# Kernel optimization log

Hardware: AMD Instinct MI355X
Metric: run time of the kernel (lower is better)

The kernel has to match this reference:

```python
import jax, jax.numpy as jnp
import numpy as np

D_MODEL = 512
N_HEADS = 8
B, T = 2, 2048
EPS = 1e-6


def _phi(x):
    # ELU feature map: elu(x) + 1 (always positive)
    return jax.nn.elu(x) + 1.0


def setup_inputs() -> dict:
    key = jax.random.key(0)
    ks = jax.random.split(key, 9)
    s = 1.0 / np.sqrt(D_MODEL)
    x = jax.random.normal(ks[0], (B, T, D_MODEL), dtype=jnp.float32)
    Wq = jax.random.uniform(ks[1], (D_MODEL, D_MODEL), jnp.float32, -s, s)
    bq = jax.random.uniform(ks[2], (D_MODEL,), jnp.float32, -s, s)
    Wk = jax.random.uniform(ks[3], (D_MODEL, D_MODEL), jnp.float32, -s, s)
    bk = jax.random.uniform(ks[4], (D_MODEL,), jnp.float32, -s, s)
    Wv = jax.random.uniform(ks[5], (D_MODEL, D_MODEL), jnp.float32, -s, s)
    bv = jax.random.uniform(ks[6], (D_MODEL,), jnp.float32, -s, s)
    Wo = jax.random.uniform(ks[7], (D_MODEL, D_MODEL), jnp.float32, -s, s)
    bo = jax.random.uniform(ks[8], (D_MODEL,), jnp.float32, -s, s)
    return {"x": x, "Wq": Wq, "bq": bq, "Wk": Wk, "bk": bk,
            "Wv": Wv, "bv": bv, "Wo": Wo, "bo": bo}


def reference(x, Wq, bq, Wk, bk, Wv, bv, Wo, bo):
    Bb, Tt, _ = x.shape
    H = N_HEADS
    D = D_MODEL // H

    def heads(W, b):
        # (B,T,d_model) -> (B,H,T,D)
        return (x @ W + b).reshape(Bb, Tt, H, D).transpose(0, 2, 1, 3)

    Q = _phi(heads(Wq, bq))
    K = _phi(heads(Wk, bk))
    V = heads(Wv, bv)

    # Causal linear attention: S_t = sum_{j<=t} phi(K_j) ⊗ V_j, z_t = sum_{j<=t} phi(K_j)
    KV = jnp.einsum('bhtd,bhtm->bhtdm', K, V)   # (B,H,T,D,D)
    S = jnp.cumsum(KV, axis=2)
    z = jnp.cumsum(K, axis=2)
    num = jnp.einsum('bhtd,bhtdm->bhtm', Q, S)  # (B,H,T,D)
    den = jnp.maximum(jnp.einsum('bhtd,bhtd->bht', Q, z), EPS)[..., None]
    out = num / den

    out = out.transpose(0, 2, 1, 3).reshape(Bb, Tt, D_MODEL)
    return out @ Wo + bo
```

## Files before the change

### kernel.cpp

```cpp
#include <hip/hip_runtime.h>
#include <math.h>

#define DM 512
#define NH 8
#define HD 64
#define BB 2
#define TT 2048
#define CHUNK 64
#define NC (TT / CHUNK)
#define BH (BB * NH)
#define ROWS (BB * TT)
#define EPSV 1e-6f

typedef short bf16x8 __attribute__((ext_vector_type(8)));
typedef float f32x4 __attribute__((ext_vector_type(4)));
typedef unsigned short us;

union U4 { us h[4]; uint2 u; };

__device__ __forceinline__ us f2bf(float f) {
    unsigned int u = __float_as_uint(f);
    return (us)((u + 0x7FFFu + ((u >> 16) & 1u)) >> 16);
}
__device__ __forceinline__ float bf2f(us h) {
    return __uint_as_float(((unsigned int)h) << 16);
}
__device__ __forceinline__ void gload16(const void* g, void* l) {
    __builtin_amdgcn_global_load_lds(
        (const __attribute__((address_space(1))) unsigned int*)g,
        (__attribute__((address_space(3))) unsigned int*)l, 16, 0, 0);
}
#define SWZ(r, k) ((k) ^ (((r) & 7) << 3))

__global__ __launch_bounds__(256) void prep(
    const float* __restrict__ x,
    const float* __restrict__ Wq, const float* __restrict__ Wk,
    const float* __restrict__ Wv, const float* __restrict__ Wo,
    us* __restrict__ xb, us* __restrict__ WT)
{
    const int bid = blockIdx.x, tid = threadIdx.x;
    __shared__ float tl[32][33];
    if (bid < 2048) {
        const int i = bid * 256 + tid;
        float4 v = ((const float4*)x)[i];
        U4 o;
        o.h[0] = f2bf(v.x); o.h[1] = f2bf(v.y);
        o.h[2] = f2bf(v.z); o.h[3] = f2bf(v.w);
        ((uint2*)xb)[i] = o.u;
    } else {
        const int b2 = bid - 2048;
        const int which = b2 >> 8, t = b2 & 255;
        const float* W = (which == 0) ? Wq : (which == 1) ? Wk : (which == 2) ? Wv : Wo;
        us* O = WT + (size_t)which * DM * DM;
        const int r0 = (t >> 4) * 32, c0 = (t & 15) * 32;
        const int tr = tid >> 3, tc = tid & 7;
        float4 v = *(const float4*)&W[(size_t)(r0 + tr) * DM + c0 + tc * 4];
        tl[tr][tc * 4 + 0] = v.x; tl[tr][tc * 4 + 1] = v.y;
        tl[tr][tc * 4 + 2] = v.z; tl[tr][tc * 4 + 3] = v.w;
        __syncthreads();
        U4 o;
#pragma unroll
        for (int i = 0; i < 4; ++i) o.h[i] = f2bf(tl[tc * 4 + i][tr]);
        *(uint2*)&O[(size_t)(c0 + tr) * DM + r0 + tc * 4] = o.u;
    }
}

__device__ __forceinline__ void stage_tiles(
    const us* __restrict__ Ag, const us* __restrict__ Bg,
    int r0, int c0, int k0, int tid, us* As, us* Bs)
{
    const int fa = tid * 8;
#pragma unroll
    for (int i = 0; i < 2; ++i) {
        const int f = fa + i * 2048, row = f >> 6, kp = f & 63;
        gload16(Ag + (size_t)(r0 + row) * DM + k0 + SWZ(row, kp), As + f);
    }
#pragma unroll
    for (int i = 0; i < 4; ++i) {
        const int f = fa + i * 2048, row = f >> 6, kp = f & 63;
        gload16(Bg + (size_t)(c0 + row) * DM + k0 + SWZ(row, kp), Bs + f);
    }
}

__device__ __forceinline__ void gemm64x128(
    const us* __restrict__ Ag, const us* __restrict__ Bg,
    int r0, int c0, int tid, us* Asl, us* Bsl, f32x4 (&acc)[2][4])
{
    const int lane = tid & 63, wid = tid >> 6;
    const int wr = wid >> 1, wc = wid & 1;
    const int lrow = lane & 15, lk8 = (lane >> 4) * 8;

    stage_tiles(Ag, Bg, r0, c0, 0, tid, Asl, Bsl);
    __syncthreads();
    int cur = 0;
    for (int k0 = 0; k0 < DM; k0 += 64) {
        if (k0 + 64 < DM)
            stage_tiles(Ag, Bg, r0, c0, k0 + 64, tid,
                        Asl + (cur ^ 1) * 4096, Bsl + (cur ^ 1) * 8192);
        const us* As = Asl + cur * 4096;
        const us* Bs = Bsl + cur * 8192;
#pragma unroll
        for (int kin = 0; kin < 64; kin += 32) {
            bf16x8 af[2], bfr[4];
#pragma unroll
            for (int mi = 0; mi < 2; ++mi) {
                const int row = wr * 32 + mi * 16 + lrow;
                af[mi] = *(const bf16x8*)&As[row * 64 + SWZ(row, kin + lk8)];
            }
#pragma unroll
            for (int ni = 0; ni < 4; ++ni) {
                const int row = wc * 64 + ni * 16 + lrow;
                bfr[ni] = *(const bf16x8*)&Bs[row * 64 + SWZ(row, kin + lk8)];
            }
#pragma unroll
            for (int mi = 0; mi < 2; ++mi)
#pragma unroll
                for (int ni = 0; ni < 4; ++ni)
                    acc[mi][ni] = __builtin_amdgcn_mfma_f32_16x16x32_bf16(
                        af[mi], bfr[ni], acc[mi][ni], 0, 0, 0);
        }
        __syncthreads();
        cur ^= 1;
    }
}

__global__ __launch_bounds__(256) void qkv_mfma(
    const us* __restrict__ xb, const us* __restrict__ WT,
    const float* __restrict__ bq, const float* __restrict__ bk,
    const float* __restrict__ bv,
    us* __restrict__ qn, us* __restrict__ kn,
    us* __restrict__ kt, us* __restrict__ vt)
{
    const int which = blockIdx.z;
    const us* Bg = WT + (size_t)which * DM * DM;
    const float* bias = (which == 0) ? bq : (which == 1) ? bk : bv;

    __shared__ us Asl[2 * 4096];
    __shared__ us Bsl[2 * 8192];
    f32x4 acc[2][4] = {};
    const int r0 = blockIdx.x * 64, c0 = blockIdx.y * 128;
    const int tid = threadIdx.x;

    gemm64x128(xb, Bg, r0, c0, tid, Asl, Bsl, acc);

    const int lane = tid & 63, wid = tid >> 6;
    const int wr = wid >> 1, wc = wid & 1;
    const int lrow = lane & 15, lr4 = (lane >> 4) * 4;
    const int b = r0 >> 11;

#pragma unroll
    for (int mi = 0; mi < 2; ++mi) {
        const int rowb = r0 + wr * 32 + mi * 16 + lr4;
        const int t0g = rowb & (TT - 1);
#pragma unroll
        for (int ni = 0; ni < 4; ++ni) {
            const int col = c0 + wc * 64 + ni * 16 + lrow;
            const int h = col >> 6, d = col & 63;
            const float bc = bias[col];
            U4 p4;
#pragma unroll
            for (int r = 0; r < 4; ++r) {
                float y = acc[mi][ni][r] + bc;
                if (which < 2) y = (y > 0.f) ? (y + 1.f) : __expf(y);
                const us hb = f2bf(y);
                p4.h[r] = hb;
                if (which == 0)
                    qn[((size_t)(b * NH + h) * TT + t0g + r) * HD + d] = hb;
                else if (which == 1)
                    kn[((size_t)(b * NH + h) * TT + t0g + r) * HD + d] = hb;
            }
            if (which == 1)
                *(uint2*)&kt[((size_t)(b * NH + h) * HD + d) * TT + t0g] = p4.u;
            else if (which == 2)
                *(uint2*)&vt[((size_t)(b * NH + h) * HD + d) * TT + t0g] = p4.u;
        }
    }
}

__global__ __launch_bounds__(256) void out_mfma(
    const us* __restrict__ Ag, const us* __restrict__ WoT,
    const float* __restrict__ bias, float* __restrict__ out)
{
    __shared__ us Asl[2 * 4096];
    __shared__ us Bsl[2 * 8192];
    f32x4 acc[2][4] = {};
    const int r0 = blockIdx.x * 64, c0 = blockIdx.y * 128;
    const int tid = threadIdx.x;

    gemm64x128(Ag, WoT, r0, c0, tid, Asl, Bsl, acc);

    const int lane = tid & 63, wid = tid >> 6;
    const int wr = wid >> 1, wc = wid & 1;
    const int lrow = lane & 15, lr4 = (lane >> 4) * 4;

#pragma unroll
    for (int mi = 0; mi < 2; ++mi)
#pragma unroll
        for (int ni = 0; ni < 4; ++ni) {
            const int col = c0 + wc * 64 + ni * 16 + lrow;
            const float bc = bias[col];
#pragma unroll
            for (int r = 0; r < 4; ++r) {
                const int row = r0 + wr * 32 + mi * 16 + lr4 + r;
                out[(size_t)row * DM + col] = acc[mi][ni][r] + bc;
            }
        }
}

__global__ __launch_bounds__(256) void chunk_sums(
    const us* __restrict__ kt, const us* __restrict__ vt,
    us* __restrict__ kvc, float* __restrict__ zc)
{
    const int blk = blockIdx.x, bh = blk >> 5, c = blk & 31;
    const int t0 = c * CHUNK;
    __shared__ us Ksl[4096], Vsl[4096];
    __shared__ float partial[4][64];
    const int tid = threadIdx.x;
    const us* ktb = kt + (size_t)bh * HD * TT;
    const us* vtb = vt + (size_t)bh * HD * TT;

#pragma unroll
    for (int i = 0; i < 2; ++i) {
        const int f = tid * 8 + i * 2048, row = f >> 6, kp = f & 63;
        const int kl = SWZ(row, kp);
        gload16(ktb + (size_t)row * TT + t0 + kl, Ksl + f);
        gload16(vtb + (size_t)row * TT + t0 + kl, Vsl + f);
    }
    __syncthreads();

    const int lane = tid & 63, wid = tid >> 6;
    const int wr = wid >> 1, wc = wid & 1;
    const int lrow = lane & 15, lk8 = (lane >> 4) * 8, lr4 = (lane >> 4) * 4;

    f32x4 acc[2][2] = {};
#pragma unroll
    for (int kin = 0; kin < 64; kin += 32) {
        bf16x8 af[2], bfr[2];
#pragma unroll
        for (int mi = 0; mi < 2; ++mi) {
            const int row = wr * 32 + mi * 16 + lrow;
            af[mi] = *(const bf16x8*)&Vsl[row * 64 + SWZ(row, kin + lk8)];
        }
#pragma unroll
        for (int ni = 0; ni < 2; ++ni) {
            const int row = wc * 32 + ni * 16 + lrow;
            bfr[ni] = *(const bf16x8*)&Ksl[row * 64 + SWZ(row, kin + lk8)];
        }
#pragma unroll
        for (int mi = 0; mi < 2; ++mi)
#pragma unroll
            for (int ni = 0; ni < 2; ++ni)
                acc[mi][ni] = __builtin_amdgcn_mfma_f32_16x16x32_bf16(
                    af[mi], bfr[ni], acc[mi][ni], 0, 0, 0);
    }

    us* dst = kvc + (size_t)blk * 4096;
#pragma unroll
    for (int mi = 0; mi < 2; ++mi)
#pragma unroll
        for (int ni = 0; ni < 2; ++ni) {
            const int d2 = wr * 32 + mi * 16 + lr4;
            const int d1 = wc * 32 + ni * 16 + lrow;
#pragma unroll
            for (int r = 0; r < 4; ++r)
                dst[(d2 + r) * 64 + d1] = f2bf(acc[mi][ni][r]);
        }

    {
        const int p = tid >> 6, d = tid & 63;
        float s = 0.f;
#pragma unroll
        for (int j = 0; j < 16; ++j)
            s += bf2f(Ksl[d * 64 + SWZ(d, p * 16 + j)]);
        partial[p][d] = s;
    }
    __syncthreads();
    if (tid < 64)
        zc[(size_t)blk * 64 + tid] =
            partial[0][tid] + partial[1][tid] + partial[2][tid] + partial[3][tid];
}

__global__ __launch_bounds__(256) void scan(
    const us* __restrict__ kvc, const float* __restrict__ zc,
    us* __restrict__ spr, float* __restrict__ zpr)
{
    const int bh = blockIdx.x, seg = blockIdx.y, tid = threadIdx.x;
    if (seg < 8) {
        const int e = seg * 512 + tid * 2;
        const size_t base = (size_t)(bh * NC) * 4096 + e;
        unsigned u[NC];
#pragma unroll
        for (int c = 0; c < NC; ++c)
            u[c] = *(const unsigned*)(kvc + base + (size_t)c * 4096);
        float r0 = 0.f, r1 = 0.f;
#pragma unroll
        for (int c = 0; c < NC; ++c) {
            const unsigned p = (unsigned)f2bf(r0) | ((unsigned)f2bf(r1) << 16);
            *(unsigned*)(spr + base + (size_t)c * 4096) = p;
            r0 += bf2f((us)(u[c] & 0xFFFF));
            r1 += bf2f((us)(u[c] >> 16));
        }
    } else if (tid < 64) {
        const size_t base = (size_t)(bh * NC) * 64 + tid;
        float zv[NC];
#pragma unroll
        for (int c = 0; c < NC; ++c) zv[c] = zc[base + (size_t)c * 64];
        float run = 0.f;
#pragma unroll
        for (int c = 0; c < NC; ++c) {
            zpr[base + (size_t)c * 64] = run;
            run += zv[c];
        }
    }
}

__global__ __launch_bounds__(256) void chunk_attn(
    const us* __restrict__ qn, const us* __restrict__ kn,
    const us* __restrict__ vt, const us* __restrict__ spr,
    const float* __restrict__ zpr, us* __restrict__ attn)
{
    const int blk = blockIdx.x, bh = blk >> 5, c = blk & 31;
    const int t0 = c * CHUNK;
    __shared__ us Qs[4096], Kns[4096], Vts[4096], Sts[4096], Abf[4096];
    __shared__ float zp[64], den[64], part[4][64];
    const int tid = threadIdx.x;

    const us* qb = qn + ((size_t)bh * TT + t0) * HD;
    const us* kb = kn + ((size_t)bh * TT + t0) * HD;
    const us* vb = vt + (size_t)bh * HD * TT;
    const us* sb = spr + (size_t)blk * 4096;

#pragma unroll
    for (int i = 0; i < 2; ++i) {
        const int f = tid * 8 + i * 2048, row = f >> 6, kp = f & 63;
        const int kl = SWZ(row, kp);
        gload16(qb + (size_t)row * HD + kl, Qs + f);
        gload16(kb + (size_t)row * HD + kl, Kns + f);
        gload16(vb + (size_t)row * TT + t0 + kl, Vts + f);
        gload16(sb + (size_t)row * 64 + kl, Sts + f);
    }
    if (tid < 64) zp[tid] = zpr[(size_t)blk * 64 + tid];
    __syncthreads();

    const int lane = tid & 63, wid = tid >> 6;
    const int wr = wid >> 1, wc = wid & 1;
    const int lrow = lane & 15, lk8 = (lane >> 4) * 8, lr4 = (lane >> 4) * 4;

    f32x4 accs[2][2] = {};
#pragma unroll
    for (int kin = 0; kin < 64; kin += 32) {
        bf16x8 af[2], bfr[2];
#pragma unroll
        for (int mi = 0; mi < 2; ++mi) {
            const int row = wr * 32 + mi * 16 + lrow;
            af[mi] = *(const bf16x8*)&Qs[row * 64 + SWZ(row, kin + lk8)];
        }
#pragma unroll
        for (int ni = 0; ni < 2; ++ni) {
            const int row = wc * 32 + ni * 16 + lrow;
            bfr[ni] = *(const bf16x8*)&Kns[row * 64 + SWZ(row, kin + lk8)];
        }
#pragma unroll
        for (int mi = 0; mi < 2; ++mi)
#pragma unroll
            for (int ni = 0; ni < 2; ++ni)
                accs[mi][ni] = __builtin_amdgcn_mfma_f32_16x16x32_bf16(
                    af[mi], bfr[ni], accs[mi][ni], 0, 0, 0);
    }

#pragma unroll
    for (int mi = 0; mi < 2; ++mi)
#pragma unroll
        for (int ni = 0; ni < 2; ++ni) {
            const int j = wc * 32 + ni * 16 + lrow;
#pragma unroll
            for (int r = 0; r < 4; ++r) {
                const int i = wr * 32 + mi * 16 + lr4 + r;
                const float v = (j <= i) ? accs[mi][ni][r] : 0.f;
                Abf[i * 64 + SWZ(i, j)] = f2bf(v);
            }
        }
    __syncthreads();

    {
        const int p = tid >> 6, i = tid & 63;
        float s = 0.f;
#pragma unroll
        for (int jj = 0; jj < 16; ++jj) {
            const int j = p * 16 + jj;
            s += bf2f(Abf[i * 64 + SWZ(i, j)]);
            s += bf2f(Qs[i * 64 + SWZ(i, j)]) * zp[j];
        }
        part[p][i] = s;
    }
    __syncthreads();
    if (tid < 64)
        den[tid] = fmaxf(part[0][tid] + part[1][tid] + part[2][tid] + part[3][tid], EPSV);
    __syncthreads();

    f32x4 acco[2][2] = {};
#pragma unroll
    for (int kin = 0; kin < 64; kin += 32) {
        bf16x8 af[2], bfr[2], ag[2], bgr[2];
#pragma unroll
        for (int mi = 0; mi < 2; ++mi) {
            const int row = wr * 32 + mi * 16 + lrow;
            af[mi] = *(const bf16x8*)&Abf[row * 64 + SWZ(row, kin + lk8)];
            ag[mi] = *(const bf16x8*)&Qs[row * 64 + SWZ(row, kin + lk8)];
        }
#pragma unroll
        for (int ni = 0; ni < 2; ++ni) {
            const int row = wc * 32 + ni * 16 + lrow;
            bfr[ni] = *(const bf16x8*)&Vts[row * 64 + SWZ(row, kin + lk8)];
            bgr[ni] = *(const bf16x8*)&Sts[row * 64 + SWZ(row, kin + lk8)];
        }
#pragma unroll
        for (int mi = 0; mi < 2; ++mi)
#pragma unroll
            for (int ni = 0; ni < 2; ++ni) {
                acco[mi][ni] = __builtin_amdgcn_mfma_f32_16x16x32_bf16(
                    af[mi], bfr[ni], acco[mi][ni], 0, 0, 0);
                acco[mi][ni] = __builtin_amdgcn_mfma_f32_16x16x32_bf16(
                    ag[mi], bgr[ni], acco[mi][ni], 0, 0, 0);
            }
    }

    const int b = bh >> 3, h = bh & 7;
#pragma unroll
    for (int mi = 0; mi < 2; ++mi)
#pragma unroll
        for (int ni = 0; ni < 2; ++ni) {
            const int d2 = wc * 32 + ni * 16 + lrow;
#pragma unroll
            for (int r = 0; r < 4; ++r) {
                const int i = wr * 32 + mi * 16 + lr4 + r;
                attn[((size_t)b * TT + t0 + i) * DM + h * HD + d2] =
                    f2bf(acco[mi][ni][r] / den[i]);
            }
        }
}

extern "C" void kernel_launch(void* const* d_in, const int* in_sizes, int n_in,
                              void* d_out, int out_size, void* d_ws, size_t ws_size,
                              hipStream_t stream)
{
    const float* x  = (const float*)d_in[0];
    const float* Wq = (const float*)d_in[1];
    const float* bq = (const float*)d_in[2];
    const float* Wk = (const float*)d_in[3];
    const float* bk = (const float*)d_in[4];
    const float* Wv = (const float*)d_in[5];
    const float* bv = (const float*)d_in[6];
    const float* Wo = (const float*)d_in[7];
    const float* bo = (const float*)d_in[8];
    float* out = (float*)d_out;

    const size_t SZ = (size_t)BH * TT * HD;
    us* xb  = (us*)d_ws;
    us* WT  = xb + SZ;
    us* qn  = WT + (size_t)4 * DM * DM;
    us* kn  = qn + SZ;
    us* kt  = kn + SZ;
    us* vt  = kt + SZ;
    us* kvc = vt + SZ;
    us* spr = kvc + SZ;
    float* zc  = (float*)(spr + SZ);
    float* zpr = zc + (size_t)BH * NC * 64;
    us* attn = xb;

    prep<<<3072, 256, 0, stream>>>(x, Wq, Wk, Wv, Wo, xb, WT);
    qkv_mfma<<<dim3(ROWS / 64, DM / 128, 3), 256, 0, stream>>>(
        xb, WT, bq, bk, bv, qn, kn, kt, vt);
    chunk_sums<<<BH * NC, 256, 0, stream>>>(kt, vt, kvc, zc);
    scan<<<dim3(BH, 9), 256, 0, stream>>>(kvc, zc, spr, zpr);
    chunk_attn<<<BH * NC, 256, 0, stream>>>(qn, kn, vt, spr, zpr, attn);
    out_mfma<<<dim3(ROWS / 64, DM / 128), 256, 0, stream>>>(
        attn, WT + (size_t)3 * DM * DM, bo, out);
}
```

Before: 49.31 us.

## Enlarge GEMM tiles, transpose K/V via LDS, and compute row sums with MFMA

The QKV and output GEMMs move from 64x128 to 128x128 tiles with a single LDS buffer, dropping the double-buffered prefetch. The K/V transposed stores are now staged through swizzled LDS so they can be written as coalesced 16-byte rows. The chunk z-sums and the attention denominators are computed with extra MFMAs against ones and z vectors, replacing the LDS reduction loops and their barriers. The larger tiles halve the grid, which lowers occupancy on a 256-CU part and loses load/compute overlap, and the z and denominator values now go through bf16 rounding, which costs some precision.

```diff
diff --git a/kernel.cpp b/kernel.cpp
--- a/kernel.cpp
+++ b/kernel.cpp
@@ -31,6 +31,7 @@
         (__attribute__((address_space(3))) unsigned int*)l, 16, 0, 0);
 }
 #define SWZ(r, k) ((k) ^ (((r) & 7) << 3))
+#define SWZ128(c, t) (((t) & 64) | (((t) & 63) ^ (((c) & 7) << 3)))
 
 __global__ __launch_bounds__(256) void prep(
     const float* __restrict__ x,
@@ -65,46 +66,30 @@
     }
 }
 
-__device__ __forceinline__ void stage_tiles(
+__device__ __forceinline__ void gemm128(
     const us* __restrict__ Ag, const us* __restrict__ Bg,
-    int r0, int c0, int k0, int tid, us* As, us* Bs)
-{
-    const int fa = tid * 8;
-#pragma unroll
-    for (int i = 0; i < 2; ++i) {
-        const int f = fa + i * 2048, row = f >> 6, kp = f & 63;
-        gload16(Ag + (size_t)(r0 + row) * DM + k0 + SWZ(row, kp), As + f);
-    }
-#pragma unroll
-    for (int i = 0; i < 4; ++i) {
-        const int f = fa + i * 2048, row = f >> 6, kp = f & 63;
-        gload16(Bg + (size_t)(c0 + row) * DM + k0 + SWZ(row, kp), Bs + f);
-    }
-}
-
-__device__ __forceinline__ void gemm64x128(
-    const us* __restrict__ Ag, const us* __restrict__ Bg,
-    int r0, int c0, int tid, us* Asl, us* Bsl, f32x4 (&acc)[2][4])
+    int r0, int c0, int tid, us* As, us* Bs, f32x4 (&acc)[4][4])
 {
     const int lane = tid & 63, wid = tid >> 6;
     const int wr = wid >> 1, wc = wid & 1;
     const int lrow = lane & 15, lk8 = (lane >> 4) * 8;
-
-    stage_tiles(Ag, Bg, r0, c0, 0, tid, Asl, Bsl);
-    __syncthreads();
-    int cur = 0;
+    const int fa = tid * 8;
+
     for (int k0 = 0; k0 < DM; k0 += 64) {
-        if (k0 + 64 < DM)
-            stage_tiles(Ag, Bg, r0, c0, k0 + 64, tid,
-                        Asl + (cur ^ 1) * 4096, Bsl + (cur ^ 1) * 8192);
-        const us* As = Asl + cur * 4096;
-        const us* Bs = Bsl + cur * 8192;
+        __syncthreads();
+#pragma unroll
+        for (int i = 0; i < 4; ++i) {
+            const int f = fa + i * 2048, row = f >> 6, kp = f & 63;
+            gload16(Ag + (size_t)(r0 + row) * DM + k0 + SWZ(row, kp), As + f);
+            gload16(Bg + (size_t)(c0 + row) * DM + k0 + SWZ(row, kp), Bs + f);
+        }
+        __syncthreads();
 #pragma unroll
         for (int kin = 0; kin < 64; kin += 32) {
-            bf16x8 af[2], bfr[4];
-#pragma unroll
-            for (int mi = 0; mi < 2; ++mi) {
-                const int row = wr * 32 + mi * 16 + lrow;
+            bf16x8 af[4], bfr[4];
+#pragma unroll
+            for (int mi = 0; mi < 4; ++mi) {
+                const int row = wr * 64 + mi * 16 + lrow;
                 af[mi] = *(const bf16x8*)&As[row * 64 + SWZ(row, kin + lk8)];
             }
 #pragma unroll
@@ -113,14 +98,12 @@
                 bfr[ni] = *(const bf16x8*)&Bs[row * 64 + SWZ(row, kin + lk8)];
             }
 #pragma unroll
-            for (int mi = 0; mi < 2; ++mi)
+            for (int mi = 0; mi < 4; ++mi)
 #pragma unroll
                 for (int ni = 0; ni < 4; ++ni)
                     acc[mi][ni] = __builtin_amdgcn_mfma_f32_16x16x32_bf16(
                         af[mi], bfr[ni], acc[mi][ni], 0, 0, 0);
         }
-        __syncthreads();
-        cur ^= 1;
     }
 }
 
@@ -135,45 +118,77 @@
     const us* Bg = WT + (size_t)which * DM * DM;
     const float* bias = (which == 0) ? bq : (which == 1) ? bk : bv;
 
-    __shared__ us Asl[2 * 4096];
-    __shared__ us Bsl[2 * 8192];
-    f32x4 acc[2][4] = {};
-    const int r0 = blockIdx.x * 64, c0 = blockIdx.y * 128;
+    __shared__ us sh[16384];
+    us* As = sh;
+    us* Bs = sh + 8192;
+    us* Cb = sh;
+
+    f32x4 acc[4][4] = {};
+    const int r0 = blockIdx.x * 128, c0 = blockIdx.y * 128;
     const int tid = threadIdx.x;
 
-    gemm64x128(xb, Bg, r0, c0, tid, Asl, Bsl, acc);
+    gemm128(xb, Bg, r0, c0, tid, As, Bs, acc);
 
     const int lane = tid & 63, wid = tid >> 6;
     const int wr = wid >> 1, wc = wid & 1;
     const int lrow = lane & 15, lr4 = (lane >> 4) * 4;
-    const int b = r0 >> 11;
-
-#pragma unroll
-    for (int mi = 0; mi < 2; ++mi) {
-        const int rowb = r0 + wr * 32 + mi * 16 + lr4;
-        const int t0g = rowb & (TT - 1);
+    const int b = r0 >> 11, t0b = r0 & (TT - 1);
+
+    if (which == 0) {
+#pragma unroll
+        for (int mi = 0; mi < 4; ++mi) {
+            const int t = t0b + wr * 64 + mi * 16 + lr4;
+#pragma unroll
+            for (int ni = 0; ni < 4; ++ni) {
+                const int col = c0 + wc * 64 + ni * 16 + lrow;
+                const int h = col >> 6, d = col & 63;
+                const float bc = bias[col];
+#pragma unroll
+                for (int r = 0; r < 4; ++r) {
+                    float y = acc[mi][ni][r] + bc;
+                    y = (y > 0.f) ? (y + 1.f) : __expf(y);
+                    qn[((size_t)(b * NH + h) * TT + t + r) * HD + d] = f2bf(y);
+                }
+            }
+        }
+        return;
+    }
+
+    __syncthreads();
+#pragma unroll
+    for (int mi = 0; mi < 4; ++mi) {
+        const int tL = wr * 64 + mi * 16 + lr4;
 #pragma unroll
         for (int ni = 0; ni < 4; ++ni) {
-            const int col = c0 + wc * 64 + ni * 16 + lrow;
-            const int h = col >> 6, d = col & 63;
+            const int colL = wc * 64 + ni * 16 + lrow;
+            const int col = c0 + colL;
             const float bc = bias[col];
             U4 p4;
 #pragma unroll
             for (int r = 0; r < 4; ++r) {
                 float y = acc[mi][ni][r] + bc;
-                if (which < 2) y = (y > 0.f) ? (y + 1.f) : __expf(y);
-                const us hb = f2bf(y);
-                p4.h[r] = hb;
-                if (which == 0)
-                    qn[((size_t)(b * NH + h) * TT + t0g + r) * HD + d] = hb;
-                else if (which == 1)
-                    kn[((size_t)(b * NH + h) * TT + t0g + r) * HD + d] = hb;
-            }
-            if (which == 1)
-                *(uint2*)&kt[((size_t)(b * NH + h) * HD + d) * TT + t0g] = p4.u;
-            else if (which == 2)
-                *(uint2*)&vt[((size_t)(b * NH + h) * HD + d) * TT + t0g] = p4.u;
-        }
+                if (which == 1) y = (y > 0.f) ? (y + 1.f) : __expf(y);
+                p4.h[r] = f2bf(y);
+            }
+            if (which == 1) {
+                const int h = col >> 6, d = col & 63;
+#pragma unroll
+                for (int r = 0; r < 4; ++r)
+                    kn[((size_t)(b * NH + h) * TT + t0b + tL + r) * HD + d] = p4.h[r];
+            }
+            *(uint2*)&Cb[colL * 128 + SWZ128(colL, tL)] = p4.u;
+        }
+    }
+    __syncthreads();
+
+    us* dst = (which == 1) ? kt : vt;
+#pragma unroll
+    for (int it = 0; it < 8; ++it) {
+        const int colL = it * 16 + wid * 4 + (lane >> 4);
+        const int tch = (lane & 15) * 8;
+        const uint4 v = *(const uint4*)&Cb[colL * 128 + SWZ128(colL, tch)];
+        const int col = c0 + colL, h = col >> 6, d = col & 63;
+        *(uint4*)&dst[((size_t)(b * NH + h) * HD + d) * TT + t0b + tch] = v;
     }
 }
 
@@ -181,27 +196,26 @@
     const us* __restrict__ Ag, const us* __restrict__ WoT,
     const float* __restrict__ bias, float* __restrict__ out)
 {
-    __shared__ us Asl[2 * 4096];
-    __shared__ us Bsl[2 * 8192];
-    f32x4 acc[2][4] = {};
-    const int r0 = blockIdx.x * 64, c0 = blockIdx.y * 128;
+    __shared__ us sh[16384];
+    f32x4 acc[4][4] = {};
+    const int r0 = blockIdx.x * 128, c0 = blockIdx.y * 128;
     const int tid = threadIdx.x;
 
-    gemm64x128(Ag, WoT, r0, c0, tid, Asl, Bsl, acc);
+    gemm128(Ag, WoT, r0, c0, tid, sh, sh + 8192, acc);
 
     const int lane = tid & 63, wid = tid >> 6;
     const int wr = wid >> 1, wc = wid & 1;
     const int lrow = lane & 15, lr4 = (lane >> 4) * 4;
 
 #pragma unroll
-    for (int mi = 0; mi < 2; ++mi)
+    for (int mi = 0; mi < 4; ++mi)
 #pragma unroll
         for (int ni = 0; ni < 4; ++ni) {
             const int col = c0 + wc * 64 + ni * 16 + lrow;
             const float bc = bias[col];
 #pragma unroll
             for (int r = 0; r < 4; ++r) {
-                const int row = r0 + wr * 32 + mi * 16 + lr4 + r;
+                const int row = r0 + wr * 64 + mi * 16 + lr4 + r;
                 out[(size_t)row * DM + col] = acc[mi][ni][r] + bc;
             }
         }
@@ -214,7 +228,6 @@
     const int blk = blockIdx.x, bh = blk >> 5, c = blk & 31;
     const int t0 = c * CHUNK;
     __shared__ us Ksl[4096], Vsl[4096];
-    __shared__ float partial[4][64];
     const int tid = threadIdx.x;
     const us* ktb = kt + (size_t)bh * HD * TT;
     const us* vtb = vt + (size_t)bh * HD * TT;
@@ -232,7 +245,13 @@
     const int wr = wid >> 1, wc = wid & 1;
     const int lrow = lane & 15, lk8 = (lane >> 4) * 8, lr4 = (lane >> 4) * 4;
 
+    bf16x8 onesA = {};
+    if (lrow == 0)
+#pragma unroll
+        for (int e = 0; e < 8; ++e) onesA[e] = (short)0x3F80;
+
     f32x4 acc[2][2] = {};
+    f32x4 accz[2] = {};
 #pragma unroll
     for (int kin = 0; kin < 64; kin += 32) {
         bf16x8 af[2], bfr[2];
@@ -252,6 +271,11 @@
             for (int ni = 0; ni < 2; ++ni)
                 acc[mi][ni] = __builtin_amdgcn_mfma_f32_16x16x32_bf16(
                     af[mi], bfr[ni], acc[mi][ni], 0, 0, 0);
+        if (wr == 0)
+#pragma unroll
+            for (int ni = 0; ni < 2; ++ni)
+                accz[ni] = __builtin_amdgcn_mfma_f32_16x16x32_bf16(
+                    onesA, bfr[ni], accz[ni], 0, 0, 0);
     }
 
     us* dst = kvc + (size_t)blk * 4096;
@@ -266,18 +290,10 @@
                 dst[(d2 + r) * 64 + d1] = f2bf(acc[mi][ni][r]);
         }
 
-    {
-        const int p = tid >> 6, d = tid & 63;
-        float s = 0.f;
-#pragma unroll
-        for (int j = 0; j < 16; ++j)
-            s += bf2f(Ksl[d * 64 + SWZ(d, p * 16 + j)]);
-        partial[p][d] = s;
-    }
-    __syncthreads();
-    if (tid < 64)
-        zc[(size_t)blk * 64 + tid] =
-            partial[0][tid] + partial[1][tid] + partial[2][tid] + partial[3][tid];
+    if (wr == 0 && lane < 16)
+#pragma unroll
+        for (int ni = 0; ni < 2; ++ni)
+            zc[(size_t)blk * 64 + wc * 32 + ni * 16 + lane] = accz[ni][0];
 }
 
 __global__ __launch_bounds__(256) void scan(
@@ -322,7 +338,7 @@
     const int blk = blockIdx.x, bh = blk >> 5, c = blk & 31;
     const int t0 = c * CHUNK;
     __shared__ us Qs[4096], Kns[4096], Vts[4096], Sts[4096], Abf[4096];
-    __shared__ float zp[64], den[64], part[4][64];
+    __shared__ float zp[64];
     const int tid = threadIdx.x;
 
     const us* qb = qn + ((size_t)bh * TT + t0) * HD;
@@ -382,31 +398,25 @@
         }
     __syncthreads();
 
-    {
-        const int p = tid >> 6, i = tid & 63;
-        float s = 0.f;
-#pragma unroll
-        for (int jj = 0; jj < 16; ++jj) {
-            const int j = p * 16 + jj;
-            s += bf2f(Abf[i * 64 + SWZ(i, j)]);
-            s += bf2f(Qs[i * 64 + SWZ(i, j)]) * zp[j];
-        }
-        part[p][i] = s;
-    }
-    __syncthreads();
-    if (tid < 64)
-        den[tid] = fmaxf(part[0][tid] + part[1][tid] + part[2][tid] + part[3][tid], EPSV);
-    __syncthreads();
+    bf16x8 onesB = {}, zB = {};
+    if (lrow == 0) {
+#pragma unroll
+        for (int e = 0; e < 8; ++e) {
+            onesB[e] = (short)0x3F80;
+            zB[e] = (short)f2bf(zp[lk8 + e]);
+        }
+    }
 
     f32x4 acco[2][2] = {};
+    f32x4 accd[2] = {};
 #pragma unroll
     for (int kin = 0; kin < 64; kin += 32) {
-        bf16x8 af[2], bfr[2], ag[2], bgr[2];
+        bf16x8 af_a[2], af_q[2], bfr[2], bgr[2];
 #pragma unroll
         for (int mi = 0; mi < 2; ++mi) {
             const int row = wr * 32 + mi * 16 + lrow;
-            af[mi] = *(const bf16x8*)&Abf[row * 64 + SWZ(row, kin + lk8)];
-            ag[mi] = *(const bf16x8*)&Qs[row * 64 + SWZ(row, kin + lk8)];
+            af_a[mi] = *(const bf16x8*)&Abf[row * 64 + SWZ(row, kin + lk8)];
+            af_q[mi] = *(const bf16x8*)&Qs[row * 64 + SWZ(row, kin + lk8)];
         }
 #pragma unroll
         for (int ni = 0; ni < 2; ++ni) {
@@ -415,15 +425,27 @@
             bgr[ni] = *(const bf16x8*)&Sts[row * 64 + SWZ(row, kin + lk8)];
         }
 #pragma unroll
-        for (int mi = 0; mi < 2; ++mi)
+        for (int mi = 0; mi < 2; ++mi) {
+            accd[mi] = __builtin_amdgcn_mfma_f32_16x16x32_bf16(
+                af_a[mi], onesB, accd[mi], 0, 0, 0);
+            accd[mi] = __builtin_amdgcn_mfma_f32_16x16x32_bf16(
+                af_q[mi], zB, accd[mi], 0, 0, 0);
 #pragma unroll
             for (int ni = 0; ni < 2; ++ni) {
                 acco[mi][ni] = __builtin_amdgcn_mfma_f32_16x16x32_bf16(
-                    af[mi], bfr[ni], acco[mi][ni], 0, 0, 0);
+                    af_a[mi], bfr[ni], acco[mi][ni], 0, 0, 0);
                 acco[mi][ni] = __builtin_amdgcn_mfma_f32_16x16x32_bf16(
-                    ag[mi], bgr[ni], acco[mi][ni], 0, 0, 0);
-            }
-    }
+                    af_q[mi], bgr[ni], acco[mi][ni], 0, 0, 0);
+            }
+        }
+    }
+
+    float denr[2][4];
+#pragma unroll
+    for (int mi = 0; mi < 2; ++mi)
+#pragma unroll
+        for (int r = 0; r < 4; ++r)
+            denr[mi][r] = fmaxf(__shfl(accd[mi][r], (int)(lane & 48), 64), EPSV);
 
     const int b = bh >> 3, h = bh & 7;
 #pragma unroll
@@ -435,7 +457,7 @@
             for (int r = 0; r < 4; ++r) {
                 const int i = wr * 32 + mi * 16 + lr4 + r;
                 attn[((size_t)b * TT + t0 + i) * DM + h * HD + d2] =
-                    f2bf(acco[mi][ni][r] / den[i]);
+                    f2bf(acco[mi][ni][r] / denr[mi][r]);
             }
         }
 }
@@ -469,11 +491,11 @@
     us* attn = xb;
 
     prep<<<3072, 256, 0, stream>>>(x, Wq, Wk, Wv, Wo, xb, WT);
-    qkv_mfma<<<dim3(ROWS / 64, DM / 128, 3), 256, 0, stream>>>(
+    qkv_mfma<<<dim3(ROWS / 128, DM / 128, 3), 256, 0, stream>>>(
         xb, WT, bq, bk, bv, qn, kn, kt, vt);
     chunk_sums<<<BH * NC, 256, 0, stream>>>(kt, vt, kvc, zc);
     scan<<<dim3(BH, 9), 256, 0, stream>>>(kvc, zc, spr, zpr);
     chunk_attn<<<BH * NC, 256, 0, stream>>>(qn, kn, vt, spr, zpr, attn);
-    out_mfma<<<dim3(ROWS / 64, DM / 128), 256, 0, stream>>>(
+    out_mfma<<<dim3(ROWS / 128, DM / 128), 256, 0, stream>>>(
         attn, WT + (size_t)3 * DM * DM, bo, out);
 }
```

After: 53.03 us. 1.08x slower.
